# Performance work log

Measured on AMD Instinct MI355X. Metric: run time of the kernel, lower is better.

Reference implementation:

```python
import jax, jax.numpy as jnp
import numpy as np

N_NODES = 200_000
N_EDGES = 6_400_000
N_GRAPHS = 512
F_IN = 92   # CGCNN atom feature dim
WIDTH = 10  # hard-coded config.width in GCNSimple
F_OUT = 1   # output_features


def setup_inputs() -> dict:
    key = jax.random.key(0)
    ks = jax.random.split(key, 10)
    atom_features = jax.random.normal(ks[0], (N_NODES, F_IN), dtype=jnp.float32)
    r = jax.random.normal(ks[1], (N_EDGES, 3), dtype=jnp.float32)
    W_emb = jax.random.normal(ks[2], (F_IN, WIDTH), dtype=jnp.float32) * 0.1
    b_emb = jax.random.normal(ks[3], (WIDTH,), dtype=jnp.float32) * 0.1
    W1 = jax.random.normal(ks[4], (WIDTH, WIDTH), dtype=jnp.float32) * 0.3
    b1 = jax.random.normal(ks[5], (WIDTH,), dtype=jnp.float32) * 0.1
    W2 = jax.random.normal(ks[6], (WIDTH, F_OUT), dtype=jnp.float32) * 0.3
    b2 = jax.random.normal(ks[7], (F_OUT,), dtype=jnp.float32) * 0.1
    src = jax.random.randint(ks[8], (N_EDGES,), 0, N_NODES, dtype=jnp.int32)
    dst = jax.random.randint(ks[9], (N_EDGES,), 0, N_NODES, dtype=jnp.int32)
    graph_ids = jnp.sort(jax.random.randint(jax.random.fold_in(key, 99), (N_NODES,), 0, N_GRAPHS, dtype=jnp.int32))
    return {
        "atom_features": atom_features, "r": r,
        "W_emb": W_emb, "b_emb": b_emb, "W1": W1, "b1": b1, "W2": W2, "b2": b2,
        "src": src, "dst": dst, "graph_ids": graph_ids, "num_graphs": N_GRAPHS,
    }


def reference(atom_features, r, W_emb, b_emb, W1, b1, W2, b2, src, dst, graph_ids, num_graphs):
    n = atom_features.shape[0]
    dt = atom_features.dtype
    # edge weights: exp(-||r||^2 / lengthscale^2), lengthscale = 1
    ew = jnp.exp(-jnp.sum(r * r, axis=1))  # [E]

    # unweighted degrees (DGL GraphConv norm='both' ignores edge_weight in norm)
    out_deg = jnp.clip(jnp.zeros(n, dt).at[src].add(1.0), 1.0)
    in_deg = jnp.clip(jnp.zeros(n, dt).at[dst].add(1.0), 1.0)
    inv_sqrt_out = out_deg ** -0.5
    inv_sqrt_in = in_deg ** -0.5

    def gconv(x, W, b, mm_first):
        # DGL GraphConv, norm='both': scale by src deg, weighted-sum aggregate,
        # scale by dst deg; weight applied before aggregation iff in > out.
        x = x * inv_sqrt_out[:, None]
        if mm_first:
            x = x @ W
        msg = x[src] * ew[:, None]                      # [E, d] gather
        agg = jax.ops.segment_sum(msg, dst, num_segments=n)  # [N, d] scatter-add
        if not mm_first:
            agg = agg @ W
        return agg * inv_sqrt_in[:, None] + b

    h = atom_features @ W_emb + b_emb                  # atom embedding [N, 10]
    x = jax.nn.relu(gconv(h, W1, b1, mm_first=False))  # 10 -> 10 (in == out: aggregate first)
    x = gconv(x, W2, b2, mm_first=True)                # 10 -> 1  (in > out: mm first)

    # AvgPooling: mean node feature per graph
    counts = jax.ops.segment_sum(jnp.ones(n, dt), graph_ids, num_segments=num_graphs)
    pooled = jax.ops.segment_sum(x, graph_ids, num_segments=num_graphs) / counts[:, None]
    return jnp.squeeze(pooled)  # [num_graphs]
```

## Files before the change

### kernel.cpp

```cpp
#include <hip/hip_runtime.h>
#include <math.h>

#define NNODES  200000
#define NEDGES  6400000
#define NGRAPHS 512
#define FIN     92
#define WID     10
#define HPAD    16
#define NBLK    ((NNODES + 255) / 256)

#define LBITS   10
#define LSIZE   1024
#define LMASK   (LSIZE - 1)
#define NB      196
#define SUBSH   7
#define SUBN    128
#define NSUB    1563
#define NSUBP   1608
#define PBLK    1280
#define EPB     (NEDGES / PBLK)
#define TILE    1250
#define NTILE   (EPB / TILE)
#define CELLS   (2 * NB)
#define CNT_N   (CELLS * PBLK)
#define SBLKS   (CNT_N / 256)
#define REF_GRID (NB * 8)

#define CHBITS  14
#define NCHK    13
#define SKEYS   (SUBN * NCHK)
#define SKPAD   1792
#define SKPT    7
#define SMAX    5120

#define AGG_THR  1024
#define AGG_GRID 512
#define GPB      (AGG_THR / 2)
#define SPIN_MAX 1536

#define LPN     8
#define LPNSH   3
#define NPB     (256 / LPN)
#define AGG_BLKS (NNODES / NPB)

__global__ void k_part_count(const int* __restrict__ src,
                             const int* __restrict__ dst,
                             int* __restrict__ cnt,
                             int* __restrict__ subcnt) {
    __shared__ int hSub[NSUB];
    __shared__ int hS[NB];
    int tid = threadIdx.x, k = blockIdx.x;
    for (int i = tid; i < NSUB; i += 256) hSub[i] = 0;
    if (tid < NB) hS[tid] = 0;
    __syncthreads();
    int base = k * EPB;
    for (int i = tid; i < EPB; i += 256) {
        int e = base + i;
        atomicAdd(&hSub[dst[e] >> SUBSH], 1);
        atomicAdd(&hS[src[e] >> LBITS], 1);
    }
    __syncthreads();
    if (tid < NB) {
        int s = 0;
        int b0 = tid * 8;
#pragma unroll
        for (int j = 0; j < 8; j++) {
            int ix = b0 + j;
            if (ix < NSUB) s += hSub[ix];
        }
        cnt[tid * PBLK + k] = s;
        cnt[(NB + tid) * PBLK + k] = hS[tid];
    }
    for (int i = tid; i < NSUB; i += 256) {
        int v = hSub[i];
        if (v) atomicAdd(&subcnt[i], v);
    }
}

__global__ void k_scan_partial(const int* __restrict__ cnt,
                               int* __restrict__ partial) {
    __shared__ int sdata[256];
    int tid = threadIdx.x;
    sdata[tid] = cnt[blockIdx.x * 256 + tid];
    __syncthreads();
    for (int s = 128; s > 0; s >>= 1) {
        if (tid < s) sdata[tid] += sdata[tid + s];
        __syncthreads();
    }
    if (tid == 0) partial[blockIdx.x] = sdata[0];
}

__global__ void k_scan_top(int* __restrict__ partial) {
    __shared__ int buf[1024];
    __shared__ int carry_s;
    if (threadIdx.x == 0) carry_s = 0;
    __syncthreads();
    for (int base = 0; base < SBLKS; base += 1024) {
        int i = base + threadIdx.x;
        int c = carry_s;
        int orig = (i < SBLKS) ? partial[i] : 0;
        buf[threadIdx.x] = orig;
        __syncthreads();
        for (int off = 1; off < 1024; off <<= 1) {
            int t = (threadIdx.x >= off) ? buf[threadIdx.x - off] : 0;
            __syncthreads();
            buf[threadIdx.x] += t;
            __syncthreads();
        }
        if (i < SBLKS) partial[i] = buf[threadIdx.x] - orig + c;
        __syncthreads();
        if (threadIdx.x == 0) carry_s = c + buf[1023];
        __syncthreads();
    }
}

__global__ void k_scan_apply(int* __restrict__ cnt,
                             const int* __restrict__ partial) {
    __shared__ int buf[256];
    int tid = threadIdx.x;
    int i = blockIdx.x * 256 + tid;
    int v = cnt[i];
    buf[tid] = v;
    __syncthreads();
    for (int off = 1; off < 256; off <<= 1) {
        int t = (tid >= off) ? buf[tid - off] : 0;
        __syncthreads();
        buf[tid] += t;
        __syncthreads();
    }
    cnt[i] = buf[tid] - v + partial[blockIdx.x];
}

__global__ void k_subscan(int* __restrict__ subcnt,
                          int* __restrict__ subcur) {
    __shared__ int sbuf[256];
    int tid = threadIdx.x;
    int vals[SKPT];
    int sum = 0;
#pragma unroll
    for (int j = 0; j < SKPT; j++) {
        int c = tid * SKPT + j;
        int v = (c < NSUB) ? subcnt[c] : 0;
        vals[j] = v;
        sum += v;
    }
    sbuf[tid] = sum;
    __syncthreads();
    for (int off = 1; off < 256; off <<= 1) {
        int t = (tid >= off) ? sbuf[tid - off] : 0;
        __syncthreads();
        sbuf[tid] += t;
        __syncthreads();
    }
    int run = sbuf[tid] - sum;
#pragma unroll
    for (int j = 0; j < SKPT; j++) {
        int c = tid * SKPT + j;
        if (c < NSUB) {
            subcnt[c] = run;
            subcur[c] = run;
            run += vals[j];
        }
    }
    if (tid == 0) subcnt[NSUB] = NEDGES;
}

__global__ void k_part_scatter(const float* __restrict__ r,
                               const int* __restrict__ src,
                               const int* __restrict__ dst,
                               const int* __restrict__ cnt,
                               float2* __restrict__ dstpart,
                               unsigned short* __restrict__ srcpart) {
    __shared__ int curD[NB], curS[NB];
    __shared__ int hD[NB], hS[NB];
    __shared__ int baseD[NB], baseS[NB];
    __shared__ int segD[NB], segS[NB];
    __shared__ int wsum[4];
    __shared__ float stW[TILE];
    __shared__ int   stK[TILE];
    __shared__ int   ddD[TILE];
    __shared__ unsigned short stS[TILE];
    __shared__ int   ddS[TILE];

    int tid = threadIdx.x, k = blockIdx.x;
    int lane = tid & 63, wv = tid >> 6;
    if (tid < NB) {
        curD[tid] = cnt[tid * PBLK + k];
        curS[tid] = cnt[(NB + tid) * PBLK + k] - NEDGES;
    }
    __syncthreads();

    int base = k * EPB;
    for (int t = 0; t < NTILE; t++) {
        int tbase = base + t * TILE;
        if (tid < NB) { hD[tid] = 0; hS[tid] = 0; }
        __syncthreads();
        for (int i = tid; i < TILE; i += 256) {
            int e = tbase + i;
            atomicAdd(&hD[dst[e] >> LBITS], 1);
            atomicAdd(&hS[src[e] >> LBITS], 1);
        }
        __syncthreads();
        {
            int v = (tid < NB) ? hD[tid] : 0;
            int x = v;
#pragma unroll
            for (int off = 1; off < 64; off <<= 1) {
                int tv = __shfl_up(x, off, 64);
                if (lane >= off) x += tv;
            }
            if (lane == 63) wsum[wv] = x;
            __syncthreads();
            if (tid == 0) {
                int a = 0;
#pragma unroll
                for (int wvi = 0; wvi < 4; wvi++) { int tv = wsum[wvi]; wsum[wvi] = a; a += tv; }
            }
            __syncthreads();
            int excl = x - v + wsum[wv];
            if (tid < NB) {
                baseD[tid] = excl;
                segD[tid] = curD[tid];
                curD[tid] += v;
                hD[tid] = excl;
            }
        }
        __syncthreads();
        {
            int v = (tid < NB) ? hS[tid] : 0;
            int x = v;
#pragma unroll
            for (int off = 1; off < 64; off <<= 1) {
                int tv = __shfl_up(x, off, 64);
                if (lane >= off) x += tv;
            }
            if (lane == 63) wsum[wv] = x;
            __syncthreads();
            if (tid == 0) {
                int a = 0;
#pragma unroll
                for (int wvi = 0; wvi < 4; wvi++) { int tv = wsum[wvi]; wsum[wvi] = a; a += tv; }
            }
            __syncthreads();
            int excl = x - v + wsum[wv];
            if (tid < NB) {
                baseS[tid] = excl;
                segS[tid] = curS[tid];
                curS[tid] += v;
                hS[tid] = excl;
            }
        }
        __syncthreads();
        for (int i = tid; i < TILE; i += 256) {
            int e = tbase + i;
            int s = src[e], d = dst[e];
            float x = r[3 * e + 0];
            float y = r[3 * e + 1];
            float z = r[3 * e + 2];
            float w = expf(-(x * x + y * y + z * z));
            int cd = d >> LBITS;
            int idx = atomicAdd(&hD[cd], 1);
            stW[idx] = w;
            stK[idx] = (s << LBITS) | (d & LMASK);
            ddD[idx] = segD[cd] + (idx - baseD[cd]);
            int cs = s >> LBITS;
            int ids = atomicAdd(&hS[cs], 1);
            stS[ids] = (unsigned short)(s & LMASK);
            ddS[ids] = segS[cs] + (ids - baseS[cs]);
        }
        __syncthreads();
        for (int i = tid; i < TILE; i += 256) {
            dstpart[ddD[i]] = make_float2(stW[i], __int_as_float(stK[i]));
            srcpart[ddS[i]] = stS[i];
        }
        __syncthreads();
    }
}

__global__ void k_bucket_odeg(const unsigned short* __restrict__ srcpart,
                              const int* __restrict__ cnt,
                              float* __restrict__ inv_out) {
    __shared__ int hist[LSIZE];
    int tid = threadIdx.x, b = blockIdx.x;
    int bstart = cnt[(NB + b) * PBLK] - NEDGES;
    int bend = (b == NB - 1) ? NEDGES : (cnt[(NB + b + 1) * PBLK] - NEDGES);
    for (int l = tid; l < LSIZE; l += 256) hist[l] = 0;
    __syncthreads();
    for (int p = bstart + tid; p < bend; p += 256)
        atomicAdd(&hist[srcpart[p]], 1);
    __syncthreads();
    for (int l = tid; l < LSIZE; l += 256) {
        int n = (b << LBITS) + l;
        if (n < NNODES) {
            int c = hist[l];
            inv_out[n] = rsqrtf((float)(c < 1 ? 1 : c));
        }
    }
}

__global__ void k_refine(const float2* __restrict__ dstpart,
                         const int* __restrict__ cnt,
                         int* __restrict__ subcur,
                         float2* __restrict__ dstfine) {
    int p = blockIdx.x >> 3;
    int q = blockIdx.x & 7;
    int bstart = cnt[p * PBLK];
    int bend = (p == NB - 1) ? NEDGES : cnt[(p + 1) * PBLK];
    int sz = bend - bstart;
    int qs = bstart + (int)(((long long)sz * q) >> 3);
    int qe = bstart + (int)(((long long)sz * (q + 1)) >> 3);
    int lane = threadIdx.x & 63;
    int wv = threadIdx.x >> 6;

    for (int base = qs + wv * 64; base < qe; base += 256) {
        int i = base + lane;
        bool act = (i < qe);
        float2 rec = make_float2(0.0f, 0.0f);
        if (act) rec = dstpart[i];
        unsigned pk = __float_as_uint(rec.y);
        int s3 = (pk >> SUBSH) & 7;
        unsigned long long b0 = __ballot(s3 & 1);
        unsigned long long b1 = __ballot(s3 & 2);
        unsigned long long b2 = __ballot(s3 & 4);
        unsigned long long am = __ballot(act);
        unsigned long long M = ((s3 & 1) ? b0 : ~b0)
                             & ((s3 & 2) ? b1 : ~b1)
                             & ((s3 & 4) ? b2 : ~b2) & am;
        if (act) {
            int cj = __popcll(M);
            int rank = __popcll(M & ((1ull << lane) - 1ull));
            int leader = __ffsll((unsigned long long)M) - 1;
            int gb = 0;
            if (lane == leader) gb = atomicAdd(&subcur[p * 8 + s3], cj);
            gb = __shfl(gb, leader, 64);
            dstfine[gb + rank] = rec;
        }
    }
}

__global__ void k_bucket_csr(float2* __restrict__ data,
                             const int* __restrict__ subscan,
                             int* __restrict__ row_ptr,
                             float* __restrict__ inv_in) {
    __shared__ int hist[SKPAD];
    __shared__ int sbuf[256];
    __shared__ float2 stout[SMAX];
    int tid = threadIdx.x;
    int sub = blockIdx.x;
    int substart = subscan[sub];
    int subend = subscan[sub + 1];
    int sz = subend - substart;

    for (int j = tid; j < SKPAD; j += 256) hist[j] = 0;
    __syncthreads();
    for (int p = substart + tid; p < subend; p += 256) {
        unsigned pk = __float_as_uint(data[p].y);
        atomicAdd(&hist[(pk & 127u) * NCHK + (pk >> 24)], 1);
    }
    __syncthreads();
    int kb = tid * SKPT;
    int sum = 0;
#pragma unroll
    for (int j = 0; j < SKPT; j++) sum += hist[kb + j];
    sbuf[tid] = sum;
    __syncthreads();
    for (int off = 1; off < 256; off <<= 1) {
        int tv = (tid >= off) ? sbuf[tid - off] : 0;
        __syncthreads();
        sbuf[tid] += tv;
        __syncthreads();
    }
    int run = sbuf[tid] - sum + substart;
#pragma unroll
    for (int j = 0; j < SKPT; j++) {
        int c = hist[kb + j];
        hist[kb + j] = run;
        run += c;
    }
    __syncthreads();
    if (tid < SUBN) {
        int l = tid;
        int rs = hist[l * NCHK];
        int re = (l == SUBN - 1) ? subend : hist[(l + 1) * NCHK];
        int n = (sub << SUBSH) + l;
        if (n < NNODES) {
            row_ptr[n] = rs;
            int c = re - rs;
            inv_in[n] = rsqrtf((float)(c < 1 ? 1 : c));
        }
    }
    __syncthreads();
    if (sz <= SMAX) {
        for (int p = substart + tid; p < subend; p += 256) {
            float2 rec = data[p];
            unsigned pk = __float_as_uint(rec.y);
            int pos = atomicAdd(&hist[(pk & 127u) * NCHK + (pk >> 24)], 1);
            stout[pos - substart] = make_float2(rec.x, __int_as_float((int)(pk >> LBITS)));
        }
        __syncthreads();
        for (int i = tid; i < sz; i += 256)
            data[substart + i] = stout[i];
    } else {
        for (int p = substart + tid; p < subend; p += 256) {
            float2 rec = data[p];
            unsigned pk = __float_as_uint(rec.y);
            int pos = atomicAdd(&hist[(pk & 127u) * NCHK + (pk >> 24)], 1);
            data[pos] = make_float2(rec.x, __int_as_float((int)(pk >> LBITS)));
        }
    }
}

__global__ void k_embed(const float* __restrict__ A,
                        const float* __restrict__ Wemb,
                        const float* __restrict__ bemb,
                        const float* __restrict__ inv_out,
                        float* __restrict__ hs) {
    __shared__ float sW[FIN * WID];
    __shared__ float sb[WID];
    for (int i = threadIdx.x; i < FIN * WID; i += blockDim.x) sW[i] = Wemb[i];
    if (threadIdx.x < WID) sb[threadIdx.x] = bemb[threadIdx.x];
    __syncthreads();

    int n = blockIdx.x * blockDim.x + threadIdx.x;
    if (n >= NNODES) return;

    float acc[WID];
#pragma unroll
    for (int k = 0; k < WID; k++) acc[k] = sb[k];

    const float4* row4 = reinterpret_cast<const float4*>(A + (size_t)n * FIN);
#pragma unroll
    for (int f4 = 0; f4 < FIN / 4; f4++) {
        float4 v = row4[f4];
        int f = f4 * 4;
#pragma unroll
        for (int k = 0; k < WID; k++) acc[k] += v.x * sW[(f + 0) * WID + k];
#pragma unroll
        for (int k = 0; k < WID; k++) acc[k] += v.y * sW[(f + 1) * WID + k];
#pragma unroll
        for (int k = 0; k < WID; k++) acc[k] += v.z * sW[(f + 2) * WID + k];
#pragma unroll
        for (int k = 0; k < WID; k++) acc[k] += v.w * sW[(f + 3) * WID + k];
    }

    float sc = inv_out[n];
    float* out = hs + (size_t)n * HPAD;
    float4 o0 = make_float4(acc[0] * sc, acc[1] * sc, acc[2] * sc, acc[3] * sc);
    float4 o1 = make_float4(acc[4] * sc, acc[5] * sc, acc[6] * sc, acc[7] * sc);
    float2 o2 = make_float2(acc[8] * sc, acc[9] * sc);
    *reinterpret_cast<float4*>(out + 0) = o0;
    *reinterpret_cast<float4*>(out + 4) = o1;
    *reinterpret_cast<float2*>(out + 8) = o2;
}

__global__ __launch_bounds__(AGG_THR, 8)
void k_agg1(const float2* __restrict__ csr,
            const int* __restrict__ row_ptr,
            const float* __restrict__ hs,
            const float* __restrict__ W1,
            const float* __restrict__ b1,
            const float* __restrict__ W2,
            const float* __restrict__ inv_in,
            const float* __restrict__ inv_out,
            int* __restrict__ bar8,
            int* __restrict__ bar,
            float* __restrict__ sproj) {
    __shared__ float sW1[WID * WID];
    __shared__ float sb1[WID];
    __shared__ float sW2[WID];
    int tid = threadIdx.x;
    for (int i = tid; i < WID * WID; i += AGG_THR) sW1[i] = W1[i];
    if (tid < WID) {
        sb1[tid] = b1[tid];
        sW2[tid] = W2[tid];
    }
    __syncthreads();

    int sub = tid & 1;
    int n = blockIdx.x * GPB + (tid >> 1);
    bool valid = (n < NNODES);
    int start = 0, end = 0;
    if (valid) {
        start = row_ptr[n];
        end = (n == NNODES - 1) ? NEDGES : row_ptr[n + 1];
    }

    float acc[WID];
#pragma unroll
    for (int k = 0; k < WID; k++) acc[k] = 0.0f;

    int p = start + sub;
    for (int c = 0; c < NCHK; c++) {
        int slim = (c + 1) << CHBITS;
        while (p < end) {
            float2 c2 = csr[p];
            int s = __float_as_int(c2.y);
            if (s >= slim) break;
            float w = c2.x;
            const float* hrow = hs + (size_t)s * HPAD;
            float4 a = *reinterpret_cast<const float4*>(hrow + 0);
            float4 b = *reinterpret_cast<const float4*>(hrow + 4);
            float2 cc = *reinterpret_cast<const float2*>(hrow + 8);
            acc[0] += w * a.x; acc[1] += w * a.y; acc[2] += w * a.z; acc[3] += w * a.w;
            acc[4] += w * b.x; acc[5] += w * b.y; acc[6] += w * b.z; acc[7] += w * b.w;
            acc[8] += w * cc.x; acc[9] += w * cc.y;
            p += 2;
        }
        if (c < NCHK - 1) {
            __syncthreads();
            if (tid == 0) {
                int a = atomicAdd(&bar8[c * 8 + (blockIdx.x & 7)], 1);
                if (a == (AGG_GRID / 8) - 1) atomicAdd(&bar[c], 1);
                int t = 0;
                while (__hip_atomic_load(&bar[c], __ATOMIC_RELAXED,
                                         __HIP_MEMORY_SCOPE_AGENT) < 8 &&
                       ++t < SPIN_MAX)
                    __builtin_amdgcn_s_sleep(2);
            }
            __syncthreads();
        }
    }
    for (; p < end; p += 2) {
        float2 c2 = csr[p];
        float w = c2.x;
        int s = __float_as_int(c2.y);
        const float* hrow = hs + (size_t)s * HPAD;
        float4 a = *reinterpret_cast<const float4*>(hrow + 0);
        float4 b = *reinterpret_cast<const float4*>(hrow + 4);
        float2 cc = *reinterpret_cast<const float2*>(hrow + 8);
        acc[0] += w * a.x; acc[1] += w * a.y; acc[2] += w * a.z; acc[3] += w * a.w;
        acc[4] += w * b.x; acc[5] += w * b.y; acc[6] += w * b.z; acc[7] += w * b.w;
        acc[8] += w * cc.x; acc[9] += w * cc.y;
    }

#pragma unroll
    for (int k = 0; k < WID; k++) acc[k] += __shfl_xor(acc[k], 1, 64);

    if (!valid || sub != 0) return;
    float ii = inv_in[n];
    float dot = 0.0f;
#pragma unroll
    for (int j = 0; j < WID; j++) {
        float y = 0.0f;
#pragma unroll
        for (int k = 0; k < WID; k++) y += acc[k] * sW1[k * WID + j];
        y = y * ii + sb1[j];
        y = y > 0.0f ? y : 0.0f;
        dot += y * sW2[j];
    }
    sproj[n] = dot * inv_out[n];
}

__global__ void k_agg2_pool(const float2* __restrict__ csr,
                            const int* __restrict__ row_ptr,
                            const float* __restrict__ sproj,
                            const float* __restrict__ inv_in,
                            const float* __restrict__ b2,
                            const int* __restrict__ graph_ids,
                            float* __restrict__ pooled) {
    int tid = threadIdx.x;
    int lane = tid & 63;
    int sub = tid & (LPN - 1);
    int n = blockIdx.x * NPB + (tid >> LPNSH);

    int start = row_ptr[n];
    int end = (n == NNODES - 1) ? NEDGES : row_ptr[n + 1];
    float sum = 0.0f;
    for (int p = start + sub; p < end; p += LPN) {
        float2 c2 = csr[p];
        sum += c2.x * sproj[__float_as_int(c2.y)];
    }
#pragma unroll
    for (int m = 1; m < LPN; m <<= 1) sum += __shfl_xor(sum, m, 64);

    float v = sum * inv_in[n] + b2[0];
    int g = graph_ids[n];

#pragma unroll
    for (int off = LPN; off < 64; off <<= 1) {
        float vv = __shfl_down(v, off, 64);
        int gg = __shfl_down(g, off, 64);
        if (lane + off < 64 && gg == g) v += vv;
    }
    int gprev = __shfl_up(g, LPN, 64);
    bool head = (sub == 0) && (lane < LPN || gprev != g);
    if (head) atomicAdd(&pooled[g], v);
}

__global__ void k_final(const float* __restrict__ pooled,
                        const int* __restrict__ gids,
                        float* __restrict__ out) {
    int g = blockIdx.x * blockDim.x + threadIdx.x;
    if (g >= NGRAPHS) return;
    int lo = 0, hi = NNODES;
    while (lo < hi) { int m = (lo + hi) >> 1; if (gids[m] < g) lo = m + 1; else hi = m; }
    int first = lo;
    hi = NNODES;
    while (lo < hi) { int m = (lo + hi) >> 1; if (gids[m] < g + 1) lo = m + 1; else hi = m; }
    int cnt = lo - first;
    out[g] = pooled[g] / (float)(cnt > 0 ? cnt : 1);
}

extern "C" void kernel_launch(void* const* d_in, const int* in_sizes, int n_in,
                              void* d_out, int out_size, void* d_ws, size_t ws_size,
                              hipStream_t stream) {
    const float* atom = (const float*)d_in[0];
    const float* r    = (const float*)d_in[1];
    const float* Wemb = (const float*)d_in[2];
    const float* bemb = (const float*)d_in[3];
    const float* W1   = (const float*)d_in[4];
    const float* b1   = (const float*)d_in[5];
    const float* W2   = (const float*)d_in[6];
    const float* b2   = (const float*)d_in[7];
    const int*   src  = (const int*)d_in[8];
    const int*   dst  = (const int*)d_in[9];
    const int*   gids = (const int*)d_in[10];
    float* out = (float*)d_out;

    char* w = (char*)d_ws;
    float* pooled  = (float*)w;  w += (size_t)NGRAPHS * 4;
    int*   barmem  = (int*)w;    w += (size_t)128 * 4;
    int*   subscan = (int*)w;    w += (size_t)NSUBP * 4;
    int*   subcur  = (int*)w;    w += (size_t)NSUBP * 4;
    int*   cnt     = (int*)w;    w += (size_t)CNT_N * 4;
    int*   partial = (int*)w;    w += (size_t)((SBLKS + 3) & ~3) * 4;
    int*   row_ptr = (int*)w;    w += (size_t)((NNODES + 4) & ~3) * 4;
    float* inv_in  = (float*)w;  w += (size_t)NNODES * 4;
    float* inv_out = (float*)w;  w += (size_t)NNODES * 4;
    float* sproj   = (float*)w;  w += (size_t)NNODES * 4;
    float* hs      = (float*)w;  w += (size_t)NNODES * HPAD * 4;
    float2* dstpart = (float2*)w; w += (size_t)NEDGES * 8;
    float2* csrbuf  = (float2*)w; w += (size_t)NEDGES * 8;
    unsigned short* srcpart = (unsigned short*)csrbuf;

    int* bar8 = barmem;
    int* bar  = barmem + 104;

    hipMemsetAsync(pooled, 0, (size_t)NGRAPHS * 4, stream);
    hipMemsetAsync(barmem, 0, (size_t)128 * 4, stream);
    hipMemsetAsync(subscan, 0, (size_t)NSUBP * 4, stream);

    const int B = 256;

    k_part_count<<<PBLK, B, 0, stream>>>(src, dst, cnt, subscan);
    k_scan_partial<<<SBLKS, B, 0, stream>>>(cnt, partial);
    k_scan_top<<<1, 1024, 0, stream>>>(partial);
    k_scan_apply<<<SBLKS, B, 0, stream>>>(cnt, partial);
    k_subscan<<<1, B, 0, stream>>>(subscan, subcur);
    k_part_scatter<<<PBLK, B, 0, stream>>>(r, src, dst, cnt, dstpart, srcpart);
    k_bucket_odeg<<<NB, B, 0, stream>>>(srcpart, cnt, inv_out);
    k_refine<<<REF_GRID, B, 0, stream>>>(dstpart, cnt, subcur, csrbuf);
    k_bucket_csr<<<NSUB, B, 0, stream>>>(csrbuf, subscan, row_ptr, inv_in);
    k_embed<<<NBLK, B, 0, stream>>>(atom, Wemb, bemb, inv_out, hs);
    k_agg1<<<AGG_GRID, AGG_THR, 0, stream>>>(csrbuf, row_ptr, hs, W1, b1, W2,
                                             inv_in, inv_out, bar8, bar, sproj);
    k_agg2_pool<<<AGG_BLKS, B, 0, stream>>>(csrbuf, row_ptr, sproj, inv_in, b2, gids, pooled);
    k_final<<<(NGRAPHS + B - 1) / B, B, 0, stream>>>(pooled, gids, out);
}
```

Measured before the change: 754.7 us.

## Precompute per-node chunk ends and cut grid barrier phases from thirteen to five

The bucket-CSR kernel now writes each node's edge end offset for every source chunk into a chend table. The first aggregation kernel uses these offsets as loop bounds instead of checking each edge's source against a chunk limit. It also groups the chunks into five phases (ending at planes 2, 5, 8, 11 and 12), so there are four soft grid barriers instead of twelve. Barrier counters are padded to separate cache lines and the spin limit is raised. This trades extra chend writes and reads, plus less tightly ordered L2 reuse of the gathered hs rows, for fewer synchronisation stalls and a simpler inner loop.

```diff
diff --git a/kernel.cpp b/kernel.cpp
--- a/kernel.cpp
+++ b/kernel.cpp
@@ -36,7 +36,8 @@
 #define AGG_THR  1024
 #define AGG_GRID 512
 #define GPB      (AGG_THR / 2)
-#define SPIN_MAX 1536
+#define NPHASE   5
+#define SPIN_MAX 4096
 
 #define LPN     8
 #define LPNSH   3
@@ -341,7 +342,8 @@
 __global__ void k_bucket_csr(float2* __restrict__ data,
                              const int* __restrict__ subscan,
                              int* __restrict__ row_ptr,
-                             float* __restrict__ inv_in) {
+                             float* __restrict__ inv_in,
+                             int* __restrict__ chend) {
     __shared__ int hist[SKPAD];
     __shared__ int sbuf[256];
     __shared__ float2 stout[SMAX];
@@ -408,6 +410,16 @@
             data[pos] = make_float2(rec.x, __int_as_float((int)(pk >> LBITS)));
         }
     }
+    __syncthreads();
+    if (tid < SUBN) {
+        int l = tid;
+        int n = (sub << SUBSH) + l;
+        if (n < NNODES) {
+#pragma unroll
+            for (int c = 0; c < NCHK; c++)
+                chend[(size_t)c * NNODES + n] = hist[l * NCHK + c];
+        }
+    }
 }
 
 __global__ void k_embed(const float* __restrict__ A,
@@ -456,14 +468,15 @@
 __global__ __launch_bounds__(AGG_THR, 8)
 void k_agg1(const float2* __restrict__ csr,
             const int* __restrict__ row_ptr,
+            const int* __restrict__ chend,
             const float* __restrict__ hs,
             const float* __restrict__ W1,
             const float* __restrict__ b1,
             const float* __restrict__ W2,
             const float* __restrict__ inv_in,
             const float* __restrict__ inv_out,
-            int* __restrict__ bar8,
-            int* __restrict__ bar,
+            int* __restrict__ barA,
+            int* __restrict__ barT,
             float* __restrict__ sproj) {
     __shared__ float sW1[WID * WID];
     __shared__ float sb1[WID];
@@ -479,24 +492,22 @@
     int sub = tid & 1;
     int n = blockIdx.x * GPB + (tid >> 1);
     bool valid = (n < NNODES);
-    int start = 0, end = 0;
-    if (valid) {
-        start = row_ptr[n];
-        end = (n == NNODES - 1) ? NEDGES : row_ptr[n + 1];
-    }
+    int p = 0;
+    if (valid) p = row_ptr[n] + sub;
 
     float acc[WID];
 #pragma unroll
     for (int k = 0; k < WID; k++) acc[k] = 0.0f;
 
-    int p = start + sub;
-    for (int c = 0; c < NCHK; c++) {
-        int slim = (c + 1) << CHBITS;
-        while (p < end) {
+#pragma unroll
+    for (int t = 0; t < NPHASE; t++) {
+        int plane = (t < 4) ? (3 * t + 2) : 12;
+        int pend = 0;
+        if (valid) pend = chend[(size_t)plane * NNODES + n];
+        for (; p < pend; p += 2) {
             float2 c2 = csr[p];
+            float w = c2.x;
             int s = __float_as_int(c2.y);
-            if (s >= slim) break;
-            float w = c2.x;
             const float* hrow = hs + (size_t)s * HPAD;
             float4 a = *reinterpret_cast<const float4*>(hrow + 0);
             float4 b = *reinterpret_cast<const float4*>(hrow + 4);
@@ -504,33 +515,21 @@
             acc[0] += w * a.x; acc[1] += w * a.y; acc[2] += w * a.z; acc[3] += w * a.w;
             acc[4] += w * b.x; acc[5] += w * b.y; acc[6] += w * b.z; acc[7] += w * b.w;
             acc[8] += w * cc.x; acc[9] += w * cc.y;
-            p += 2;
-        }
-        if (c < NCHK - 1) {
+        }
+        if (t < NPHASE - 1) {
             __syncthreads();
             if (tid == 0) {
-                int a = atomicAdd(&bar8[c * 8 + (blockIdx.x & 7)], 1);
-                if (a == (AGG_GRID / 8) - 1) atomicAdd(&bar[c], 1);
-                int t = 0;
-                while (__hip_atomic_load(&bar[c], __ATOMIC_RELAXED,
+                int g = blockIdx.x & 7;
+                int a = atomicAdd(&barA[(t * 8 + g) * 16], 1);
+                if (a == (AGG_GRID / 8) - 1) atomicAdd(&barT[t * 16], 1);
+                int cnt = 0;
+                while (__hip_atomic_load(&barT[t * 16], __ATOMIC_RELAXED,
                                          __HIP_MEMORY_SCOPE_AGENT) < 8 &&
-                       ++t < SPIN_MAX)
+                       ++cnt < SPIN_MAX)
                     __builtin_amdgcn_s_sleep(2);
             }
             __syncthreads();
         }
-    }
-    for (; p < end; p += 2) {
-        float2 c2 = csr[p];
-        float w = c2.x;
-        int s = __float_as_int(c2.y);
-        const float* hrow = hs + (size_t)s * HPAD;
-        float4 a = *reinterpret_cast<const float4*>(hrow + 0);
-        float4 b = *reinterpret_cast<const float4*>(hrow + 4);
-        float2 cc = *reinterpret_cast<const float2*>(hrow + 8);
-        acc[0] += w * a.x; acc[1] += w * a.y; acc[2] += w * a.z; acc[3] += w * a.w;
-        acc[4] += w * b.x; acc[5] += w * b.y; acc[6] += w * b.z; acc[7] += w * b.w;
-        acc[8] += w * cc.x; acc[9] += w * cc.y;
     }
 
 #pragma unroll
@@ -619,12 +618,13 @@
 
     char* w = (char*)d_ws;
     float* pooled  = (float*)w;  w += (size_t)NGRAPHS * 4;
-    int*   barmem  = (int*)w;    w += (size_t)128 * 4;
+    int*   barmem  = (int*)w;    w += (size_t)1024 * 4;
     int*   subscan = (int*)w;    w += (size_t)NSUBP * 4;
     int*   subcur  = (int*)w;    w += (size_t)NSUBP * 4;
     int*   cnt     = (int*)w;    w += (size_t)CNT_N * 4;
     int*   partial = (int*)w;    w += (size_t)((SBLKS + 3) & ~3) * 4;
     int*   row_ptr = (int*)w;    w += (size_t)((NNODES + 4) & ~3) * 4;
+    int*   chend   = (int*)w;    w += (size_t)NNODES * NCHK * 4;
     float* inv_in  = (float*)w;  w += (size_t)NNODES * 4;
     float* inv_out = (float*)w;  w += (size_t)NNODES * 4;
     float* sproj   = (float*)w;  w += (size_t)NNODES * 4;
@@ -633,11 +633,11 @@
     float2* csrbuf  = (float2*)w; w += (size_t)NEDGES * 8;
     unsigned short* srcpart = (unsigned short*)csrbuf;
 
-    int* bar8 = barmem;
-    int* bar  = barmem + 104;
+    int* barA = barmem;
+    int* barT = barmem + 512;
 
     hipMemsetAsync(pooled, 0, (size_t)NGRAPHS * 4, stream);
-    hipMemsetAsync(barmem, 0, (size_t)128 * 4, stream);
+    hipMemsetAsync(barmem, 0, (size_t)1024 * 4, stream);
     hipMemsetAsync(subscan, 0, (size_t)NSUBP * 4, stream);
 
     const int B = 256;
@@ -650,10 +650,10 @@
     k_part_scatter<<<PBLK, B, 0, stream>>>(r, src, dst, cnt, dstpart, srcpart);
     k_bucket_odeg<<<NB, B, 0, stream>>>(srcpart, cnt, inv_out);
     k_refine<<<REF_GRID, B, 0, stream>>>(dstpart, cnt, subcur, csrbuf);
-    k_bucket_csr<<<NSUB, B, 0, stream>>>(csrbuf, subscan, row_ptr, inv_in);
+    k_bucket_csr<<<NSUB, B, 0, stream>>>(csrbuf, subscan, row_ptr, inv_in, chend);
     k_embed<<<NBLK, B, 0, stream>>>(atom, Wemb, bemb, inv_out, hs);
-    k_agg1<<<AGG_GRID, AGG_THR, 0, stream>>>(csrbuf, row_ptr, hs, W1, b1, W2,
-                                             inv_in, inv_out, bar8, bar, sproj);
+    k_agg1<<<AGG_GRID, AGG_THR, 0, stream>>>(csrbuf, row_ptr, chend, hs, W1, b1, W2,
+                                             inv_in, inv_out, barA, barT, sproj);
     k_agg2_pool<<<AGG_BLKS, B, 0, stream>>>(csrbuf, row_ptr, sproj, inv_in, b2, gids, pooled);
     k_final<<<(NGRAPHS + B - 1) / B, B, 0, stream>>>(pooled, gids, out);
 }
```

Measured after the change: 712.7 us. 5.6% less time.
